# Optimization experiments

Measured on AMD Instinct MI355X. Metric: run time of the kernel, lower is better.

## Reference

```python
import jax, jax.numpy as jnp
import numpy as np

D_MODEL = 1024
N_HEADS = 16
D_K = D_MODEL // N_HEADS
B, S = 2, 2048


def setup_inputs() -> dict:
    key = jax.random.key(0)
    ks = jax.random.split(key, 12)
    s = 1.0 / np.sqrt(D_MODEL)
    inp = {
        "query": jax.random.normal(ks[0], (B, S, D_MODEL), jnp.float32),
        "key": jax.random.normal(ks[1], (B, S, D_MODEL), jnp.float32),
        "value": jax.random.normal(ks[2], (B, S, D_MODEL), jnp.float32),
        "W_q": jax.random.uniform(ks[3], (D_MODEL, D_MODEL), jnp.float32, -s, s),
        "b_q": jnp.zeros((D_MODEL,), jnp.float32),
        "W_k": jax.random.uniform(ks[4], (D_MODEL, D_MODEL), jnp.float32, -s, s),
        "b_k": jnp.zeros((D_MODEL,), jnp.float32),
        "W_v": jax.random.uniform(ks[5], (D_MODEL, D_MODEL), jnp.float32, -s, s),
        "b_v": jnp.zeros((D_MODEL,), jnp.float32),
        "W_o": jax.random.uniform(ks[6], (D_MODEL, D_MODEL), jnp.float32, -s, s),
        "b_o": jnp.zeros((D_MODEL,), jnp.float32),
        "ln_gamma": jnp.ones((D_MODEL,), jnp.float32),
        "ln_beta": jnp.zeros((D_MODEL,), jnp.float32),
    }
    return inp


def _layer_norm(x, gamma, beta, eps=1e-5):
    mu = jnp.mean(x, axis=-1, keepdims=True)
    var = jnp.var(x, axis=-1, keepdims=True)
    return (x - mu) * jax.lax.rsqrt(var + eps) * gamma + beta


def reference(query, key, value, W_q, b_q, W_k, b_k, W_v, b_v, W_o, b_o, ln_gamma, ln_beta):
    b, s, _ = query.shape
    # projections -> [b, h, s, d_k]
    q = (query @ W_q.T + b_q).reshape(b, s, N_HEADS, D_K).transpose(0, 2, 1, 3)
    k = (key @ W_k.T + b_k).reshape(b, s, N_HEADS, D_K).transpose(0, 2, 1, 3)
    v = (value @ W_v.T + b_v).reshape(b, s, N_HEADS, D_K).transpose(0, 2, 1, 3)
    # scaled dot-product attention (no mask)
    scores = jnp.einsum('bhqd,bhkd->bhqk', q, k) / jnp.sqrt(jnp.float32(D_K))
    attn = jax.nn.softmax(scores, axis=-1)
    ctx = jnp.einsum('bhqk,bhkd->bhqd', attn, v)  # [b,h,s,d_k]
    ctx = ctx.transpose(0, 2, 1, 3).reshape(b, s, D_MODEL)
    out = ctx @ W_o.T + b_o
    # residual uses the PROJECTED query (quirk of original module); dropout=identity (eval)
    resid = q.transpose(0, 2, 1, 3).reshape(b, s, D_MODEL)
    return _layer_norm(out + resid, ln_gamma, ln_beta)
```

## Files before the change

kernel.cpp:

```cpp
#include <hip/hip_runtime.h>

#define DM 1024
#define NH 16
#define DKq 64
#define BB 2
#define SS 2048
#define MTOT 4096

#define K2f 0.18033688011112042f
#define IK2f 5.545177444479562f

typedef __attribute__((ext_vector_type(4))) float f32x4;
typedef __attribute__((ext_vector_type(16))) float f32x16;
typedef __attribute__((ext_vector_type(8))) short s16x8;
typedef __attribute__((ext_vector_type(4))) short s16x4;
typedef __attribute__((ext_vector_type(4))) unsigned short u16x4;

__device__ __forceinline__ unsigned short f2bf(float f) {
    unsigned u = __float_as_uint(f);
    u += 0x7fff + ((u >> 16) & 1);
    return (unsigned short)(u >> 16);
}

__device__ __forceinline__ float bf2f(unsigned short x) {
    return __uint_as_float((unsigned)x << 16);
}

__device__ __forceinline__ s16x8 cvt8(f32x4 a, f32x4 b) {
    s16x8 r;
    r[0] = (short)f2bf(a[0]); r[1] = (short)f2bf(a[1]);
    r[2] = (short)f2bf(a[2]); r[3] = (short)f2bf(a[3]);
    r[4] = (short)f2bf(b[0]); r[5] = (short)f2bf(b[1]);
    r[6] = (short)f2bf(b[2]); r[7] = (short)f2bf(b[3]);
    return r;
}

__device__ __forceinline__ unsigned pkp(float a, float b) {
    return __builtin_amdgcn_perm(__float_as_uint(b), __float_as_uint(a), 0x07060302u);
}

__device__ __forceinline__ void gload_lds16(const void* g, void* l) {
    __builtin_amdgcn_global_load_lds(
        (const __attribute__((address_space(1))) unsigned int*)g,
        (__attribute__((address_space(3))) unsigned int*)l,
        16, 0, 0);
}

__global__ __launch_bounds__(256)
void cvt_kernel(const float* __restrict__ s0, const float* __restrict__ s1,
                const float* __restrict__ s2, const float* __restrict__ s3,
                const float* __restrict__ s4, const float* __restrict__ s5,
                const float* __restrict__ s6,
                unsigned short* __restrict__ Xb, unsigned short* __restrict__ Wb)
{
    const int seg = blockIdx.y;
    const float* src;
    unsigned short* dst;
    int n;
    if (seg < 3) {
        src = (seg == 0) ? s0 : (seg == 1) ? s1 : s2;
        dst = Xb + (size_t)seg * (MTOT * DM);
        n = MTOT * DM;
    } else {
        src = (seg == 3) ? s3 : (seg == 4) ? s4 : (seg == 5) ? s5 : s6;
        dst = Wb + (size_t)(seg - 3) * (DM * DM);
        n = DM * DM;
    }
    const int stride = gridDim.x * 256;
    for (int i = blockIdx.x * 256 + threadIdx.x; i * 8 < n; i += stride) {
        f32x4 a = *(const f32x4*)(src + (size_t)i * 8);
        f32x4 b = *(const f32x4*)(src + (size_t)i * 8 + 4);
        *(s16x8*)(dst + (size_t)i * 8) = cvt8(a, b);
    }
}

__global__ __launch_bounds__(256, 3)
void proj_kernel(const unsigned short* __restrict__ Xb,
                 const unsigned short* __restrict__ Wb,
                 const float* __restrict__ bq, const float* __restrict__ bk,
                 const float* __restrict__ bv,
                 unsigned short* __restrict__ Qh, unsigned short* __restrict__ Kh,
                 unsigned short* __restrict__ Vt)
{
    const int bid = blockIdx.x;
    const int t   = (bid & 7) * 96 + (bid >> 3);
    const int z   = t >> 8;
    const int ty  = (t >> 3) & 31;
    const int tx  = t & 7;

    const unsigned short* X = Xb + (size_t)z * (MTOT * DM);
    const unsigned short* W = Wb + (size_t)z * (DM * DM);
    const float* bias = (z == 0) ? bq : (z == 1) ? bk : bv;

    const int m0 = ty * 128;
    const int n0 = tx * 128;
    const int tid  = threadIdx.x;
    const int lane = tid & 63;
    const int w    = tid >> 6;
    const int wm   = w >> 1, wn = w & 1;

    __shared__ __align__(16) short lA[2][128 * 32];
    __shared__ __align__(16) short lB[2][128 * 32];

    f32x4 acc[4][4];
#pragma unroll
    for (int i = 0; i < 4; i++)
#pragma unroll
        for (int j = 0; j < 4; j++) acc[i][j] = (f32x4)(0.f);

    const int srow16 = lane >> 2;
    const int scg    = lane & 3;

#define PSTAGE(BUF, KC) {                                                     \
    const int k0_ = (KC) * 32;                                                \
    _Pragma("unroll")                                                         \
    for (int p = 0; p < 2; ++p) {                                             \
        int c = w * 2 + p;                                                    \
        int row = c * 16 + srow16;                                            \
        int kc = scg ^ ((row >> 1) & 3);                                      \
        gload_lds16(X + (size_t)(m0 + row) * DM + k0_ + kc * 8,               \
                    (char*)lA[BUF] + c * 1024);                               \
        gload_lds16(W + (size_t)(n0 + row) * DM + k0_ + kc * 8,               \
                    (char*)lB[BUF] + c * 1024);                               \
    } }

#define PCOMPUTE(BUF) {                                                       \
    s16x8 af[4], bf[4];                                                       \
    const int kq = lane >> 4;                                                 \
    _Pragma("unroll")                                                         \
    for (int i = 0; i < 4; i++) {                                             \
        int row = wm * 64 + i * 16 + (lane & 15);                             \
        int slot = kq ^ ((row >> 1) & 3);                                     \
        af[i] = *(const s16x8*)((const char*)lA[BUF] + row * 64 + slot * 16); \
    }                                                                         \
    _Pragma("unroll")                                                         \
    for (int i = 0; i < 4; i++) {                                             \
        int row = wn * 64 + i * 16 + (lane & 15);                             \
        int slot = kq ^ ((row >> 1) & 3);                                     \
        bf[i] = *(const s16x8*)((const char*)lB[BUF] + row * 64 + slot * 16); \
    }                                                                         \
    _Pragma("unroll")                                                         \
    for (int i = 0; i < 4; i++)                                               \
        _Pragma("unroll")                                                     \
        for (int j = 0; j < 4; j++)                                           \
            acc[i][j] = __builtin_amdgcn_mfma_f32_16x16x32_bf16(              \
                af[i], bf[j], acc[i][j], 0, 0, 0);                            \
    }

    PSTAGE(0, 0);
    __syncthreads();
    for (int kp = 0; kp < 16; ++kp) {
        const int k2 = kp * 2;
        if (k2 + 1 < 32) PSTAGE(1, k2 + 1);
        PCOMPUTE(0);
        __syncthreads();
        if (k2 + 2 < 32) PSTAGE(0, k2 + 2);
        PCOMPUTE(1);
        __syncthreads();
    }
#undef PSTAGE
#undef PCOMPUTE

#pragma unroll
    for (int i = 0; i < 4; i++) {
#pragma unroll
        for (int j = 0; j < 4; j++) {
            int rg0 = m0 + wm * 64 + i * 16 + 4 * (lane >> 4);
            int cg  = n0 + wn * 64 + j * 16 + (lane & 15);
            int b = rg0 >> 11, s0 = rg0 & 2047, h = cg >> 6, d = cg & 63;
            float bv_ = bias[cg];
            if (z == 2) {
                int s0p = (s0 & ~12) | ((s0 & 4) << 1) | ((s0 & 8) >> 1);
                u16x4 st;
#pragma unroll
                for (int e = 0; e < 4; e++) st[e] = f2bf(acc[i][j][e] + bv_);
                *(u16x4*)&Vt[(((size_t)(b * NH + h)) * DKq + d) * SS + s0p] = st;
            } else if (z == 0) {
#pragma unroll
                for (int e = 0; e < 4; e++)
                    Qh[(((size_t)(b * NH + h)) * SS + s0 + e) * DKq + d] =
                        f2bf((acc[i][j][e] + bv_) * K2f);
            } else {
#pragma unroll
                for (int e = 0; e < 4; e++)
                    Kh[(((size_t)(b * NH + h)) * SS + s0 + e) * DKq + d] =
                        f2bf(acc[i][j][e] + bv_);
            }
        }
    }
}

__device__ __forceinline__ void attn_tile32(
    const char* __restrict__ lkc, const char* __restrict__ lvc,
    const s16x8* aq, int l31, int hi,
    f32x16& o0, f32x16& o1, float& rs)
{
    f32x16 s0 = (f32x16)(0.f), s1 = (f32x16)(0.f);
    const int sw = (l31 & 7) << 4;
    __builtin_amdgcn_s_setprio(1);
#pragma unroll
    for (int kkd = 0; kkd < 4; kkd++) {
        const int byte = (32 * kkd + 16 * hi) ^ sw;
        s16x8 ak0 = *(const s16x8*)(lkc + l31 * 128 + byte);
        s0 = __builtin_amdgcn_mfma_f32_32x32x16_bf16(ak0, aq[kkd], s0, 0, 0, 0);
        s16x8 ak1 = *(const s16x8*)(lkc + (32 + l31) * 128 + byte);
        s1 = __builtin_amdgcn_mfma_f32_32x32x16_bf16(ak1, aq[kkd], s1, 0, 0, 0);
    }
    __builtin_amdgcn_s_setprio(0);

    float r0 = 0.f, r1 = 0.f;
#pragma unroll
    for (int r = 0; r < 16; r++) {
        float p0 = __builtin_amdgcn_exp2f(s0[r]);
        float p1 = __builtin_amdgcn_exp2f(s1[r]);
        s0[r] = p0; s1[r] = p1;
        r0 += p0; r1 += p1;
    }
    rs += r0 + r1;

    __builtin_amdgcn_s_setprio(1);
#pragma unroll
    for (int jb = 0; jb < 2; jb++) {
#pragma unroll
        for (int u = 0; u < 2; u++) {
            const int t = 2 * jb + u;
            union { unsigned uu[4]; s16x8 v; } bp;
            if (jb == 0) {
                bp.uu[0] = pkp(s0[8*u+0], s0[8*u+1]);
                bp.uu[1] = pkp(s0[8*u+2], s0[8*u+3]);
                bp.uu[2] = pkp(s0[8*u+4], s0[8*u+5]);
                bp.uu[3] = pkp(s0[8*u+6], s0[8*u+7]);
            } else {
                bp.uu[0] = pkp(s1[8*u+0], s1[8*u+1]);
                bp.uu[1] = pkp(s1[8*u+2], s1[8*u+3]);
                bp.uu[2] = pkp(s1[8*u+4], s1[8*u+5]);
                bp.uu[3] = pkp(s1[8*u+6], s1[8*u+7]);
            }
            const int vbyte = (32 * t + 16 * hi) ^ sw;
            s16x8 av0 = *(const s16x8*)(lvc + l31 * 128 + vbyte);
            o0 = __builtin_amdgcn_mfma_f32_32x32x16_bf16(av0, bp.v, o0, 0, 0, 0);
            s16x8 av1 = *(const s16x8*)(lvc + (32 + l31) * 128 + vbyte);
            o1 = __builtin_amdgcn_mfma_f32_32x32x16_bf16(av1, bp.v, o1, 0, 0, 0);
        }
    }
    __builtin_amdgcn_s_setprio(0);
}

__global__ __launch_bounds__(256)
void attn_kernel(const unsigned short* __restrict__ Qh,
                 const unsigned short* __restrict__ Kh,
                 const unsigned short* __restrict__ Vt,
                 unsigned short* __restrict__ Ctx)
{
    const int bid = blockIdx.x;
    const int tt  = (bid & 7) * 64 + (bid >> 3);
    const int bh  = tt >> 4;
    const int q0  = (tt & 15) * 128;

    const int tid = threadIdx.x, lane = tid & 63, w = tid >> 6;
    const int b = bh >> 4, h = bh & 15;
    const int l31 = lane & 31;
    const int hi  = lane >> 5;

    __shared__ __align__(16) short lKs[2][128 * 64];
    __shared__ __align__(16) short lVs[2][128 * 64];

    const size_t qk_base = (size_t)bh * SS * DKq;
    const size_t vt_base = (size_t)bh * DKq * SS;

    s16x8 aq[4];
    const int qrow = q0 + 32 * w + l31;
    {
        const unsigned short* qp = Qh + qk_base + (size_t)qrow * DKq + 8 * hi;
#pragma unroll
        for (int kkd = 0; kkd < 4; kkd++)
            aq[kkd] = *(const s16x8*)(qp + 16 * kkd);
    }

    f32x16 o0 = (f32x16)(0.f), o1 = (f32x16)(0.f);
    float rs = 0.f;

    const int lrow = lane >> 3;
    const int lcg  = (lane & 7) ^ lrow;

#define STAGE(BUF, KV0) {                                                     \
    char* dk = (char*)lKs[BUF]; char* dv = (char*)lVs[BUF];                   \
    _Pragma("unroll")                                                         \
    for (int p = 0; p < 4; ++p) {                                             \
        int c = 4 * w + p;                                         \
        int half = c >> 3, cc = c & 7;                                        \
        gload_lds16(Kh + qk_base + (size_t)((KV0) + c * 8 + lrow) * DKq + lcg * 8, \
                    dk + c * 1024);                                           \
        gload_lds16(Vt + vt_base + (size_t)(cc * 8 + lrow) * SS                \
                        + (KV0) + half * 64 + lcg * 8,                        \
                    dv + c * 1024);                                           \
    } }

    STAGE(0, 0);
    __syncthreads();

    for (int th = 0; th < 8; ++th) {
        const int T0 = th * 2;
        STAGE(1, (T0 + 1) * 128);
        attn_tile32((const char*)lKs[0], (const char*)lVs[0], aq, l31, hi, o0, o1, rs);
        attn_tile32((const char*)lKs[0] + 8192, (const char*)lVs[0] + 8192, aq, l31, hi, o0, o1, rs);
        __syncthreads();
        if (T0 + 2 < 16) STAGE(0, (T0 + 2) * 128);
        attn_tile32((const char*)lKs[1], (const char*)lVs[1], aq, l31, hi, o0, o1, rs);
        attn_tile32((const char*)lKs[1] + 8192, (const char*)lVs[1] + 8192, aq, l31, hi, o0, o1, rs);
        __syncthreads();
    }
#undef STAGE

    rs += __shfl_xor(rs, 32);
    const float inv = 1.0f / rs;
    unsigned short* crow = Ctx + ((size_t)(b * SS + qrow)) * DM + h * 64;
#pragma unroll
    for (int db = 0; db < 2; db++) {
#pragma unroll
        for (int v = 0; v < 4; v++) {
            u16x4 st;
#pragma unroll
            for (int e = 0; e < 4; e++) {
                float x = (db == 0) ? o0[4 * v + e] : o1[4 * v + e];
                st[e] = f2bf(x * inv);
            }
            *(u16x4*)(crow + 32 * db + 8 * v + 4 * hi) = st;
        }
    }
}

__global__ __launch_bounds__(256)
void outproj_kernel(const unsigned short* __restrict__ Ctx,
                    const unsigned short* __restrict__ Wo,
                    const float* __restrict__ bo,
                    const unsigned short* __restrict__ Qh,
                    float* __restrict__ Out)
{
    const int bid = blockIdx.x;
    const int t   = (bid & 7) * 32 + (bid >> 3);
    const int ty  = t >> 3;
    const int tx  = t & 7;

    const int m0 = ty * 128;
    const int n0 = tx * 128;
    const int tid = threadIdx.x, lane = tid & 63, w = tid >> 6;
    const int wm = w >> 1, wn = w & 1;

    __shared__ __align__(16) short lA[2][128 * 64];
    __shared__ __align__(16) short lB[2][128 * 64];

    f32x4 acc[4][4];
#pragma unroll
    for (int i = 0; i < 4; i++)
#pragma unroll
        for (int j = 0; j < 4; j++) acc[i][j] = (f32x4)(0.f);

    const int lrow = lane >> 3;
    const int lcg  = (lane & 7) ^ lrow;

#define PSTAGE(BUF, KT) {                                                     \
    const int k0_ = (KT) * 64;                                                \
    _Pragma("unroll")                                                         \
    for (int p = 0; p < 4; ++p) {                                             \
        int c = w * 4 + p;                                                    \
        int row = c * 8 + lrow;                                               \
        gload_lds16(Ctx + (size_t)(m0 + row) * DM + k0_ + lcg * 8,            \
                    (char*)lA[BUF] + c * 1024);                               \
        gload_lds16(Wo + (size_t)(n0 + row) * DM + k0_ + lcg * 8,             \
                    (char*)lB[BUF] + c * 1024);                               \
    } }

#define PCOMPUTE(BUF) {                                                       \
    _Pragma("unroll")                                                         \
    for (int kk = 0; kk < 2; ++kk) {                                          \
        s16x8 af[4], bf[4];                                                   \
        _Pragma("unroll")                                                     \
        for (int i = 0; i < 4; i++) {                                         \
            int row = wm * 64 + i * 16 + (lane & 15);                         \
            int byte = (kk * 64 + 16 * (lane >> 4)) ^ ((row & 7) << 4);       \
            af[i] = *(const s16x8*)((const char*)lA[BUF] + row * 128 + byte); \
        }                                                                     \
        _Pragma("unroll")                                                     \
        for (int i = 0; i < 4; i++) {                                         \
            int row = wn * 64 + i * 16 + (lane & 15);                         \
            int byte = (kk * 64 + 16 * (lane >> 4)) ^ ((row & 7) << 4);       \
            bf[i] = *(const s16x8*)((const char*)lB[BUF] + row * 128 + byte); \
        }                                                                     \
        _Pragma("unroll")                                                     \
        for (int i = 0; i < 4; i++)                                           \
            _Pragma("unroll")                                                 \
            for (int j = 0; j < 4; j++)                                       \
                acc[i][j] = __builtin_amdgcn_mfma_f32_16x16x32_bf16(          \
                    af[i], bf[j], acc[i][j], 0, 0, 0);                        \
    } }

    PSTAGE(0, 0);
    __syncthreads();
    for (int kh = 0; kh < 8; ++kh) {
        const int k0 = kh * 2;
        if (k0 + 1 < 16) PSTAGE(1, k0 + 1);
        PCOMPUTE(0);
        __syncthreads();
        if (k0 + 2 < 16) PSTAGE(0, k0 + 2);
        PCOMPUTE(1);
        __syncthreads();
    }
#undef PSTAGE
#undef PCOMPUTE

#pragma unroll
    for (int i = 0; i < 4; i++) {
#pragma unroll
        for (int j = 0; j < 4; j++) {
            int rg0 = m0 + wm * 64 + i * 16 + 4 * (lane >> 4);
            int cg  = n0 + wn * 64 + j * 16 + (lane & 15);
            int b = rg0 >> 11, s0 = rg0 & 2047, h = cg >> 6, d = cg & 63;
            float bo_ = bo[cg];
#pragma unroll
            for (int e = 0; e < 4; e++) {
                float res = bf2f(Qh[(((size_t)(b * NH + h)) * SS + s0 + e) * DKq + d]);
                Out[(size_t)(rg0 + e) * DM + cg] =
                    __builtin_fmaf(res, IK2f, acc[i][j][e] + bo_);
            }
        }
    }
}

__global__ __launch_bounds__(256)
void ln_kernel(float* __restrict__ Out, const float* __restrict__ gamma,
               const float* __restrict__ beta)
{
    const int row = blockIdx.x;
    float* rp = Out + (size_t)row * DM;
    const int tid = threadIdx.x;

    f32x4 x = *(const f32x4*)(rp + tid * 4);
    float s  = x[0] + x[1] + x[2] + x[3];
    float sq = x[0] * x[0] + x[1] * x[1] + x[2] * x[2] + x[3] * x[3];
#pragma unroll
    for (int off = 1; off < 64; off <<= 1) {
        s  += __shfl_xor(s, off);
        sq += __shfl_xor(sq, off);
    }
    __shared__ float ps[4], pq[4];
    const int w = tid >> 6;
    if ((tid & 63) == 0) { ps[w] = s; pq[w] = sq; }
    __syncthreads();
    float ts = ps[0] + ps[1] + ps[2] + ps[3];
    float tq = pq[0] + pq[1] + pq[2] + pq[3];
    float mu  = ts * (1.f / 1024.f);
    float var = tq * (1.f / 1024.f) - mu * mu;
    float rst = rsqrtf(var + 1e-5f);

    f32x4 g  = *(const f32x4*)(gamma + tid * 4);
    f32x4 bt = *(const f32x4*)(beta + tid * 4);
    f32x4 y;
#pragma unroll
    for (int e = 0; e < 4; e++) y[e] = (x[e] - mu) * rst * g[e] + bt[e];
    *(f32x4*)(rp + tid * 4) = y;
}

extern "C" void kernel_launch(void* const* d_in, const int* in_sizes, int n_in,
                              void* d_out, int out_size, void* d_ws, size_t ws_size,
                              hipStream_t stream)
{
    const float* query = (const float*)d_in[0];
    const float* key   = (const float*)d_in[1];
    const float* value = (const float*)d_in[2];
    const float* Wq = (const float*)d_in[3];
    const float* bq = (const float*)d_in[4];
    const float* Wk = (const float*)d_in[5];
    const float* bk = (const float*)d_in[6];
    const float* Wv = (const float*)d_in[7];
    const float* bv = (const float*)d_in[8];
    const float* Wo = (const float*)d_in[9];
    const float* bo = (const float*)d_in[10];
    const float* gamma = (const float*)d_in[11];
    const float* beta  = (const float*)d_in[12];

    char* ws = (char*)d_ws;
    unsigned short* Xb  = (unsigned short*)(ws);
    unsigned short* Wb  = (unsigned short*)(ws + (24u << 20));
    unsigned short* Qh  = (unsigned short*)(ws + (32u << 20));
    unsigned short* Kh  = (unsigned short*)(ws + (40u << 20));
    unsigned short* Vt  = (unsigned short*)(ws + (48u << 20));
    unsigned short* Ctx = (unsigned short*)(ws);
    float* Out = (float*)d_out;

    cvt_kernel<<<dim3(256, 7), 256, 0, stream>>>(query, key, value,
                                                 Wq, Wk, Wv, Wo, Xb, Wb);
    proj_kernel<<<768, 256, 0, stream>>>(Xb, Wb, bq, bk, bv, Qh, Kh, Vt);
    attn_kernel<<<512, 256, 0, stream>>>(Qh, Kh, Vt, Ctx);
    outproj_kernel<<<256, 256, 0, stream>>>(Ctx, Wb + 3u * DM * DM, bo, Qh, Out);
    ln_kernel<<<4096, 256, 0, stream>>>(Out, gamma, beta);
}
```

Before: 129.5 us.

## Store projected Q transposed per head to vectorize epilogue writes and residual reads

Q is now written in a head-transposed [b,h,d,s] layout, so the projection epilogue does one 4-element vector store per fragment and the out-projection residual read becomes one vector load instead of four scalar strided accesses. In exchange, the attention kernel must gather its Q fragments with 32 scalar strided loads per lane instead of 4 vector loads. That is a one-time cost per block, but it is uncoalesced.

New measurement: 131.2 us. About the same (+1.3%).

```diff
diff --git a/kernel.cpp b/kernel.cpp
--- a/kernel.cpp
+++ b/kernel.cpp
@@ -79,7 +79,7 @@
                  const unsigned short* __restrict__ Wb,
                  const float* __restrict__ bq, const float* __restrict__ bk,
                  const float* __restrict__ bv,
-                 unsigned short* __restrict__ Qh, unsigned short* __restrict__ Kh,
+                 unsigned short* __restrict__ Qt, unsigned short* __restrict__ Kh,
                  unsigned short* __restrict__ Vt)
 {
     const int bid = blockIdx.x;
@@ -176,10 +176,10 @@
                 for (int e = 0; e < 4; e++) st[e] = f2bf(acc[i][j][e] + bv_);
                 *(u16x4*)&Vt[(((size_t)(b * NH + h)) * DKq + d) * SS + s0p] = st;
             } else if (z == 0) {
-#pragma unroll
-                for (int e = 0; e < 4; e++)
-                    Qh[(((size_t)(b * NH + h)) * SS + s0 + e) * DKq + d] =
-                        f2bf((acc[i][j][e] + bv_) * K2f);
+                u16x4 st;
+#pragma unroll
+                for (int e = 0; e < 4; e++) st[e] = f2bf((acc[i][j][e] + bv_) * K2f);
+                *(u16x4*)&Qt[(((size_t)(b * NH + h)) * DKq + d) * SS + s0] = st;
             } else {
 #pragma unroll
                 for (int e = 0; e < 4; e++)
@@ -247,7 +247,7 @@
 }
 
 __global__ __launch_bounds__(256)
-void attn_kernel(const unsigned short* __restrict__ Qh,
+void attn_kernel(const unsigned short* __restrict__ Qt,
                  const unsigned short* __restrict__ Kh,
                  const unsigned short* __restrict__ Vt,
                  unsigned short* __restrict__ Ctx)
@@ -271,10 +271,13 @@
     s16x8 aq[4];
     const int qrow = q0 + 32 * w + l31;
     {
-        const unsigned short* qp = Qh + qk_base + (size_t)qrow * DKq + 8 * hi;
-#pragma unroll
-        for (int kkd = 0; kkd < 4; kkd++)
-            aq[kkd] = *(const s16x8*)(qp + 16 * kkd);
+        const unsigned short* qp = Qt + vt_base + (size_t)(8 * hi) * SS + qrow;
+#pragma unroll
+        for (int kkd = 0; kkd < 4; kkd++) {
+#pragma unroll
+            for (int j = 0; j < 8; j++)
+                aq[kkd][j] = (short)qp[(size_t)(16 * kkd + j) * SS];
+        }
     }
 
     f32x16 o0 = (f32x16)(0.f), o1 = (f32x16)(0.f);
@@ -334,7 +337,7 @@
 void outproj_kernel(const unsigned short* __restrict__ Ctx,
                     const unsigned short* __restrict__ Wo,
                     const float* __restrict__ bo,
-                    const unsigned short* __restrict__ Qh,
+                    const unsigned short* __restrict__ Qt,
                     float* __restrict__ Out)
 {
     const int bid = blockIdx.x;
@@ -417,11 +420,11 @@
             int cg  = n0 + wn * 64 + j * 16 + (lane & 15);
             int b = rg0 >> 11, s0 = rg0 & 2047, h = cg >> 6, d = cg & 63;
             float bo_ = bo[cg];
+            u16x4 rq = *(const u16x4*)&Qt[(((size_t)(b * NH + h)) * DKq + d) * SS + s0];
 #pragma unroll
             for (int e = 0; e < 4; e++) {
-                float res = bf2f(Qh[(((size_t)(b * NH + h)) * SS + s0 + e) * DKq + d]);
                 Out[(size_t)(rg0 + e) * DM + cg] =
-                    __builtin_fmaf(res, IK2f, acc[i][j][e] + bo_);
+                    __builtin_fmaf(bf2f(rq[e]), IK2f, acc[i][j][e] + bo_);
             }
         }
     }
@@ -482,7 +485,7 @@
     char* ws = (char*)d_ws;
     unsigned short* Xb  = (unsigned short*)(ws);
     unsigned short* Wb  = (unsigned short*)(ws + (24u << 20));
-    unsigned short* Qh  = (unsigned short*)(ws + (32u << 20));
+    unsigned short* Qt  = (unsigned short*)(ws + (32u << 20));
     unsigned short* Kh  = (unsigned short*)(ws + (40u << 20));
     unsigned short* Vt  = (unsigned short*)(ws + (48u << 20));
     unsigned short* Ctx = (unsigned short*)(ws);
@@ -490,8 +493,8 @@
 
     cvt_kernel<<<dim3(256, 7), 256, 0, stream>>>(query, key, value,
                                                  Wq, Wk, Wv, Wo, Xb, Wb);
-    proj_kernel<<<768, 256, 0, stream>>>(Xb, Wb, bq, bk, bv, Qh, Kh, Vt);
-    attn_kernel<<<512, 256, 0, stream>>>(Qh, Kh, Vt, Ctx);
-    outproj_kernel<<<256, 256, 0, stream>>>(Ctx, Wb + 3u * DM * DM, bo, Qh, Out);
+    proj_kernel<<<768, 256, 0, stream>>>(Xb, Wb, bq, bk, bv, Qt, Kh, Vt);
+    attn_kernel<<<512, 256, 0, stream>>>(Qt, Kh, Vt, Ctx);
+    outproj_kernel<<<256, 256, 0, stream>>>(Ctx, Wb + 3u * DM * DM, bo, Qt, Out);
     ln_kernel<<<4096, 256, 0, stream>>>(Out, gamma, beta);
 }
```
